# Optimization experiments

Hardware: AMD Instinct MI355X
Metric: run time of the kernel (lower is better)

## Reference

```python
import jax, jax.numpy as jnp
import numpy as np
from jax import lax

DT = 0.001
DX = 0.02
H = 2048
P = 256


def _lap(u):
    # 5-point Laplacian numerator on interior: u[2:,1:-1]-4u[1:-1,1:-1]+u[:-2,1:-1]+u[1:-1,2:]+u[1:-1,:-2]
    return (u[:, :, 2:, 1:-1] - 4.0 * u[:, :, 1:-1, 1:-1] + u[:, :, :-2, 1:-1]
            + u[:, :, 1:-1, 2:] + u[:, :, 1:-1, :-2])


def setup_inputs() -> dict:
    key = jax.random.key(0)
    ks = jax.random.split(key, 8)
    inp = {
        "ref_speed": jax.random.uniform(ks[0], (1, 1, H, H), jnp.float32, 0.1, 1.0),
        "batch": jax.random.normal(ks[1], (12, 1, H, H), jnp.float32),
        "x_tt": jax.random.normal(ks[2], (1, 1, H, H), jnp.float32),
        "x_t": jax.random.normal(ks[3], (1, 1, H, H), jnp.float32),
        "ref_sol": jax.random.normal(ks[4], (16, 1, H, H), jnp.float32),
        "conv_v": jax.random.normal(ks[5], (1, 3, 3, 3), jnp.float32) * np.sqrt(1.0 / (3 * 3 * 320)),
        "conv_g": jax.random.uniform(ks[6], (1,), jnp.float32, 0.5, 1.5),
        "conv_b": jax.random.normal(ks[7], (1,), jnp.float32) * 0.01,
        "loc_x": jax.random.randint(jax.random.fold_in(key, 10), (P,), 0, H),
        "loc_y": jax.random.randint(jax.random.fold_in(key, 11), (P,), 0, H),
        "bsize": 10,
        "id": 1,
        "flag": 1,
        "flag_num": 1,
    }
    return inp


def reference(ref_speed, batch, x_tt, x_t, ref_sol, conv_v, conv_g, conv_b,
              loc_x, loc_y, bsize, id, flag, flag_num):
    sg = lax.stop_gradient
    ntb = flag - 1
    step = flag_num - 1

    xtt = sg(batch[ntb * bsize + step: ntb * bsize + step + 1])   # [1,1,H,W]
    xt = sg(batch[ntb * bsize + step + 1: ntb * bsize + step + 2])

    coef = sg(ref_speed[:, :, 1:-1, 1:-1]) ** 2 * (DT ** 2) / (DX ** 2)

    # explicit FD step (outputs3)
    x_t4 = jnp.zeros_like(xt)
    x_t4 = x_t4.at[:, :, 1:-1, 1:-1].set(
        2.0 * xt[:, :, 1:-1, 1:-1] - xtt[:, :, 1:-1, 1:-1] + _lap(xt) * coef)

    # weight-normed 3x3 conv (3->1 channels, padding=1)
    vnorm = jnp.sqrt(jnp.sum(conv_v ** 2, axis=(1, 2, 3), keepdims=True))
    W = conv_g.reshape(-1, 1, 1, 1) * conv_v / vnorm
    x_t1 = jnp.concatenate([xtt, xt, ref_speed], axis=1)  # [1,3,H,W]
    y = lax.conv_general_dilated(x_t1, W, (1, 1), ((1, 1), (1, 1)),
                                 dimension_numbers=("NCHW", "OIHW", "NCHW"))
    y = y + conv_b.reshape(1, -1, 1, 1)

    # stencil update on conv output interior (RHS evaluated from pre-assignment y)
    x7 = y.at[:, :, 1:-1, 1:-1].set(
        2.0 * xt[:, :, 1:-1, 1:-1] - xtt[:, :, 1:-1, 1:-1] + _lap(y) * coef)
    x7_pre = x7  # clone captured into outputs2 before boundary edits

    # boundaries, in original order
    x7 = x7.at[:, :, 0, :].set(0.0)
    left = xt[:, :, :, 0:1] - DT * sg(ref_speed[:, :, :, 0:1]) * (xt[:, :, :, 0:1] - xt[:, :, :, 1:2]) / DX
    x7 = x7.at[:, :, :, 0:1].set(left)
    rows = jnp.arange(1, H - 1)
    cols = H - rows
    x7 = x7.at[:, :, rows, cols].set(xt[:, :, rows - 1, cols - 1])
    right = xt[:, :, :, -1:] - DT * sg(ref_speed[:, :, :, -1:]) * (xt[:, :, :, -1:] - xt[:, :, :, -2:-1]) / DX
    x7 = x7.at[:, :, :, -1:].set(right)
    x7 = x7.at[:, :, -1, :].set(0.0)

    # per-point observation scatter from ref_sol (-1 entries skipped)
    obs = ref_sol[id * bsize + step + 2: id * bsize + step + 3]  # [1,1,H,W]
    valid = loc_x != -1
    lx = jnp.where(valid, loc_x, 0)
    ly = jnp.where(valid, loc_y, 0)
    vals = obs[:, :, lx, ly]          # [1,1,P]
    cur = x7[:, :, lx, ly]
    x7 = x7.at[:, :, lx, ly].set(jnp.where(valid[None, None, :], vals, cur))

    outputs1 = jnp.concatenate([x_tt, x_t, x7], axis=0)       # [3,1,H,W]
    outputs2 = jnp.concatenate([x_tt, x_t, x7_pre], axis=0)   # [3,1,H,W]
    return jnp.concatenate([outputs1, outputs2, x_t4], axis=0)  # [7,1,H,W]
```

## Files before the change

### kernel.cpp

```cpp
#include <hip/hip_runtime.h>

#define HD   2048
#define HHW  (HD*HD)
#define TX   64
#define TY   32
#define XSTR 68
#define XROWS 36
#define YROWS 34
#define YCOLS 66


__global__ __launch_bounds__(256) void fused_kernel(
    const float* __restrict__ batch,
    const float* __restrict__ rs,
    const float* __restrict__ x_tt_in,
    const float* __restrict__ x_t_in,
    const float* __restrict__ conv_v,
    const float* __restrict__ conv_g,
    const float* __restrict__ conv_b,
    const int* __restrict__ p_bsize,
    const int* __restrict__ p_flag,
    const int* __restrict__ p_flagnum,
    float* __restrict__ out)
{
    __shared__ float xts[XROWS * XSTR];
    __shared__ float ys [YROWS * XSTR];

    const int tid = threadIdx.x;
    const int gi0 = blockIdx.y * TY;
    const int gj0 = blockIdx.x * TX;

    const int base = ((p_flag[0] - 1) * p_bsize[0] + (p_flagnum[0] - 1)) * HHW;
    const float* __restrict__ xtt = batch + base;
    const float* __restrict__ xt  = batch + base + HHW;

    float w[27];
    float ss = 0.f;
    #pragma unroll
    for (int k = 0; k < 27; ++k) { w[k] = conv_v[k]; ss += w[k] * w[k]; }
    const float scale = conv_g[0] / sqrtf(ss);
    const float bias  = conv_b[0];

    for (int p = tid; p < XROWS * XSTR; p += 256) {
        int li = p / XSTR;
        int lj = p - li * XSTR;
        int gi = gi0 - 2 + li;
        int gj = gj0 - 2 + lj;
        float v = 0.f;
        if ((unsigned)gi < HD && (unsigned)gj < HD) v = xt[gi * HD + gj];
        xts[p] = v;
    }
    __syncthreads();

    for (int p = tid; p < YROWS * YCOLS; p += 256) {
        int li = p / YCOLS;
        int lj = p - li * YCOLS;
        int gi = gi0 - 1 + li;
        int gj = gj0 - 1 + lj;
        if ((unsigned)gi >= HD || (unsigned)gj >= HD) continue;
        float acc = 0.f;
        #pragma unroll
        for (int kh = 0; kh < 3; ++kh) {
            int ii = gi + kh - 1;
            bool rok = (unsigned)ii < HD;
            const float* rowt = xtt + ii * HD;
            const float* rowr = rs  + ii * HD;
            #pragma unroll
            for (int kw = 0; kw < 3; ++kw) {
                int jj = gj + kw - 1;
                bool ok = rok && ((unsigned)jj < HD);
                float t0 = ok ? rowt[jj] : 0.f;
                float t1 = xts[(li + kh) * XSTR + lj + kw];
                float t2 = ok ? rowr[jj] : 0.f;
                acc += w[kh * 3 + kw]      * t0
                     + w[9 + kh * 3 + kw]  * t1
                     + w[18 + kh * 3 + kw] * t2;
            }
        }
        ys[li * XSTR + lj] = bias + scale * acc;
    }
    __syncthreads();

    const int c  = tid & 63;
    const int rg = tid >> 6;
    for (int k = 0; k < 8; ++k) {
        int row = rg * 8 + k;
        int gi  = gi0 + row;
        int gj  = gj0 + c;
        int idx = gi * HD + gj;

        float a_tt = x_tt_in[idx];
        float a_t  = x_t_in[idx];
        float xc = xts[(row + 2) * XSTR + c + 2];
        float xo = xtt[idx];
        float rc = rs[idx];
        float yc = ys[(row + 1) * XSTR + c + 1];

        bool interior = (gi > 0) & (gi < HD - 1) & (gj > 0) & (gj < HD - 1);
        float xt4 = 0.f, ypre;
        if (interior) {
            float coef = rc * rc * 0.0025f;
            float lapx = xts[(row + 1) * XSTR + c + 2] + xts[(row + 3) * XSTR + c + 2]
                       + xts[(row + 2) * XSTR + c + 1] + xts[(row + 2) * XSTR + c + 3] - 4.f * xc;
            xt4 = 2.f * xc - xo + lapx * coef;
            float lapy = ys[row * XSTR + c + 1] + ys[(row + 2) * XSTR + c + 1]
                       + ys[(row + 1) * XSTR + c] + ys[(row + 1) * XSTR + c + 2] - 4.f * yc;
            ypre = 2.f * xc - xo + lapy * coef;
        } else {
            ypre = yc;
        }

        float v = ypre;
        if (gi == 0) v = 0.f;
        if (gj == 0)      v = xc - 0.05f * rc * (xc - xts[(row + 2) * XSTR + 3]);
        if (gi >= 1 && gi <= HD - 2 && gj == HD - gi)
                          v = xts[(row + 1) * XSTR + c + 1];
        if (gj == HD - 1) v = xc - 0.05f * rc * (xc - xts[(row + 2) * XSTR + c + 1]);
        if (gi == HD - 1) v = 0.f;

        out[idx]            = a_tt;
        out[HHW + idx]      = a_t;
        out[2 * HHW + idx]  = v;
        out[3 * HHW + idx]  = a_tt;
        out[4 * HHW + idx]  = a_t;
        out[5 * HHW + idx]  = ypre;
        out[6 * HHW + idx]  = xt4;
    }
}

__global__ __launch_bounds__(256) void scatter_kernel(
    const float* __restrict__ ref_sol,
    const int* __restrict__ loc_x,
    const int* __restrict__ loc_y,
    const int* __restrict__ p_bsize,
    const int* __restrict__ p_id,
    const int* __restrict__ p_flagnum,
    float* __restrict__ out)
{
    int k = blockIdx.x * blockDim.x + threadIdx.x;
    if (k >= 256) return;
    int lx = loc_x[k];
    if (lx == -1) return;
    int ly = loc_y[k];
    int off = (p_id[0] * p_bsize[0] + (p_flagnum[0] - 1) + 2) * HHW;
    out[2 * HHW + lx * HD + ly] = ref_sol[off + lx * HD + ly];
}

extern "C" void kernel_launch(void* const* d_in, const int* in_sizes, int n_in,
                              void* d_out, int out_size, void* d_ws, size_t ws_size,
                              hipStream_t stream) {
    const float* ref_speed = (const float*)d_in[0];
    const float* batch     = (const float*)d_in[1];
    const float* x_tt      = (const float*)d_in[2];
    const float* x_t       = (const float*)d_in[3];
    const float* ref_sol   = (const float*)d_in[4];
    const float* conv_v    = (const float*)d_in[5];
    const float* conv_g    = (const float*)d_in[6];
    const float* conv_b    = (const float*)d_in[7];
    const int*   loc_x     = (const int*)d_in[8];
    const int*   loc_y     = (const int*)d_in[9];
    const int*   bsize     = (const int*)d_in[10];
    const int*   id        = (const int*)d_in[11];
    const int*   flag      = (const int*)d_in[12];
    const int*   flag_num  = (const int*)d_in[13];

    float* out = (float*)d_out;

    dim3 block(256);
    dim3 grid(HD / TX, HD / TY);

    fused_kernel<<<grid, block, 0, stream>>>(batch, ref_speed, x_tt, x_t,
                                             conv_v, conv_g, conv_b,
                                             bsize, flag, flag_num, out);
    scatter_kernel<<<1, 256, 0, stream>>>(ref_sol, loc_x, loc_y, bsize, id, flag_num, out);
}
```

Before: 492.1 us.

## Stage all three input tiles in LDS and vectorize with float4

The xtt and ref_speed halo tiles are now staged in shared memory alongside xt, using float4 global loads. The conv and stencil then read only from LDS, and each thread computes four outputs. Output stores also become float4, and launch bounds request 4 blocks per SM. This cuts redundant global reads in the 3x3 conv and improves memory coalescing, at the cost of more LDS per block, which may limit occupancy.

```diff
diff --git a/kernel.cpp b/kernel.cpp
--- a/kernel.cpp
+++ b/kernel.cpp
@@ -4,13 +4,14 @@
 #define HHW  (HD*HD)
 #define TX   64
 #define TY   32
-#define XSTR 68
-#define XROWS 36
-#define YROWS 34
-#define YCOLS 66
-
-
-__global__ __launch_bounds__(256) void fused_kernel(
+#define S    72
+#define XR   36
+#define YR   34
+
+
+union V4 { float4 v; float f[4]; };
+
+__global__ __launch_bounds__(256, 4) void fused_kernel(
     const float* __restrict__ batch,
     const float* __restrict__ rs,
     const float* __restrict__ x_tt_in,
@@ -23,8 +24,10 @@
     const int* __restrict__ p_flagnum,
     float* __restrict__ out)
 {
-    __shared__ float xts[XROWS * XSTR];
-    __shared__ float ys [YROWS * XSTR];
+    __shared__ float sT[XR * S];
+    __shared__ float sX[XR * S];
+    __shared__ float sR[XR * S];
+    __shared__ float sY[YR * S];
 
     const int tid = threadIdx.x;
     const int gi0 = blockIdx.y * TY;
@@ -41,90 +44,142 @@
     const float scale = conv_g[0] / sqrtf(ss);
     const float bias  = conv_b[0];
 
-    for (int p = tid; p < XROWS * XSTR; p += 256) {
-        int li = p / XSTR;
-        int lj = p - li * XSTR;
-        int gi = gi0 - 2 + li;
-        int gj = gj0 - 2 + lj;
-        float v = 0.f;
-        if ((unsigned)gi < HD && (unsigned)gj < HD) v = xt[gi * HD + gj];
-        xts[p] = v;
-    }
+#define STAGE(DST, SRC)                                                     \
+    for (int i = tid; i < XR * 18; i += 256) {                              \
+        const int r  = i / 18;                                              \
+        const int cc = i - r * 18;                                          \
+        const int gi = gi0 - 2 + r;                                         \
+        const int gj = gj0 - 4 + (cc << 2);                                 \
+        float4 val = make_float4(0.f, 0.f, 0.f, 0.f);                       \
+        if ((unsigned)gi < (unsigned)HD && (unsigned)gj <= (unsigned)(HD-4))\
+            val = *(const float4*)(SRC + gi * HD + gj);                     \
+        *(float4*)&DST[r * S + (cc << 2)] = val;                            \
+    }
+
+    STAGE(sT, xtt)
+    STAGE(sX, xt)
+    STAGE(sR, rs)
+#undef STAGE
     __syncthreads();
 
-    for (int p = tid; p < YROWS * YCOLS; p += 256) {
-        int li = p / YCOLS;
-        int lj = p - li * YCOLS;
-        int gi = gi0 - 1 + li;
-        int gj = gj0 - 1 + lj;
-        if ((unsigned)gi >= HD || (unsigned)gj >= HD) continue;
+#define ACC9(SB, WB) {                                                      \
+        V4 a, b, c;                                                         \
+        a.v = *(const float4*)&SB[o - 4];                                   \
+        b.v = *(const float4*)&SB[o];                                       \
+        c.v = *(const float4*)&SB[o + 4];                                   \
+        const float w0 = w[WB], w1 = w[WB + 1], w2 = w[WB + 2];             \
+        ax += w0 * a.f[3] + w1 * b.f[0] + w2 * b.f[1];                      \
+        ay += w0 * b.f[0] + w1 * b.f[1] + w2 * b.f[2];                      \
+        az += w0 * b.f[1] + w1 * b.f[2] + w2 * b.f[3];                      \
+        aw += w0 * b.f[2] + w1 * b.f[3] + w2 * c.f[0];                      \
+    }
+
+    for (int t = tid; t < 34 * 16; t += 256) {
+        const int row = t >> 4;
+        const int ljc = ((t & 15) << 2) + 4;
+        float ax = 0.f, ay = 0.f, az = 0.f, aw = 0.f;
+        #pragma unroll
+        for (int kh = 0; kh < 3; ++kh) {
+            const int o = (row + kh) * S + ljc;
+            ACC9(sT, kh * 3)
+            ACC9(sX, 9 + kh * 3)
+            ACC9(sR, 18 + kh * 3)
+        }
+        V4 r4;
+        r4.f[0] = bias + scale * ax;
+        r4.f[1] = bias + scale * ay;
+        r4.f[2] = bias + scale * az;
+        r4.f[3] = bias + scale * aw;
+        *(float4*)&sY[row * S + ljc] = r4.v;
+    }
+#undef ACC9
+
+    if (tid < 68) {
+        const int row = tid >> 1;
+        const int lj  = (tid & 1) ? 68 : 3;
         float acc = 0.f;
         #pragma unroll
         for (int kh = 0; kh < 3; ++kh) {
-            int ii = gi + kh - 1;
-            bool rok = (unsigned)ii < HD;
-            const float* rowt = xtt + ii * HD;
-            const float* rowr = rs  + ii * HD;
-            #pragma unroll
-            for (int kw = 0; kw < 3; ++kw) {
-                int jj = gj + kw - 1;
-                bool ok = rok && ((unsigned)jj < HD);
-                float t0 = ok ? rowt[jj] : 0.f;
-                float t1 = xts[(li + kh) * XSTR + lj + kw];
-                float t2 = ok ? rowr[jj] : 0.f;
-                acc += w[kh * 3 + kw]      * t0
-                     + w[9 + kh * 3 + kw]  * t1
-                     + w[18 + kh * 3 + kw] * t2;
-            }
+            const int o = (row + kh) * S + lj;
+            acc += w[kh*3+0]      * sT[o-1] + w[kh*3+1]      * sT[o] + w[kh*3+2]      * sT[o+1];
+            acc += w[9+kh*3+0]    * sX[o-1] + w[9+kh*3+1]    * sX[o] + w[9+kh*3+2]    * sX[o+1];
+            acc += w[18+kh*3+0]   * sR[o-1] + w[18+kh*3+1]   * sR[o] + w[18+kh*3+2]   * sR[o+1];
         }
-        ys[li * XSTR + lj] = bias + scale * acc;
+        sY[row * S + lj] = bias + scale * acc;
     }
     __syncthreads();
 
-    const int c  = tid & 63;
-    const int rg = tid >> 6;
-    for (int k = 0; k < 8; ++k) {
-        int row = rg * 8 + k;
-        int gi  = gi0 + row;
-        int gj  = gj0 + c;
-        int idx = gi * HD + gj;
-
-        float a_tt = x_tt_in[idx];
-        float a_t  = x_t_in[idx];
-        float xc = xts[(row + 2) * XSTR + c + 2];
-        float xo = xtt[idx];
-        float rc = rs[idx];
-        float yc = ys[(row + 1) * XSTR + c + 1];
-
-        bool interior = (gi > 0) & (gi < HD - 1) & (gj > 0) & (gj < HD - 1);
-        float xt4 = 0.f, ypre;
-        if (interior) {
-            float coef = rc * rc * 0.0025f;
-            float lapx = xts[(row + 1) * XSTR + c + 2] + xts[(row + 3) * XSTR + c + 2]
-                       + xts[(row + 2) * XSTR + c + 1] + xts[(row + 2) * XSTR + c + 3] - 4.f * xc;
-            xt4 = 2.f * xc - xo + lapx * coef;
-            float lapy = ys[row * XSTR + c + 1] + ys[(row + 2) * XSTR + c + 1]
-                       + ys[(row + 1) * XSTR + c] + ys[(row + 1) * XSTR + c + 2] - 4.f * yc;
-            ypre = 2.f * xc - xo + lapy * coef;
-        } else {
-            ypre = yc;
+    const int c4 = (tid & 15) << 2;
+    const int r0 = tid >> 4;
+    #pragma unroll
+    for (int pass = 0; pass < 2; ++pass) {
+        const int row = r0 + (pass << 4);
+        const int gi  = gi0 + row;
+        const int gjb = gj0 + c4;
+        const int idx = gi * HD + gjb;
+
+        V4 att, at4;
+        att.v = *(const float4*)(x_tt_in + idx);
+        at4.v = *(const float4*)(x_t_in  + idx);
+
+        const int xb = (row + 2) * S + c4 + 4;
+        V4 xc, xu, xd, xl, xr_, xo, rc;
+        xc.v  = *(const float4*)&sX[xb];
+        xu.v  = *(const float4*)&sX[xb - S];
+        xd.v  = *(const float4*)&sX[xb + S];
+        xl.v  = *(const float4*)&sX[xb - 4];
+        xr_.v = *(const float4*)&sX[xb + 4];
+        xo.v  = *(const float4*)&sT[xb];
+        rc.v  = *(const float4*)&sR[xb];
+
+        const int yb = (row + 1) * S + c4 + 4;
+        V4 yc, yu, yd, yl, yr_;
+        yc.v  = *(const float4*)&sY[yb];
+        yu.v  = *(const float4*)&sY[yb - S];
+        yd.v  = *(const float4*)&sY[yb + S];
+        yl.v  = *(const float4*)&sY[yb - 4];
+        yr_.v = *(const float4*)&sY[yb + 4];
+
+        const bool gi_int = (gi >= 1) && (gi <= HD - 2);
+        V4 o2, o5, o6;
+        #pragma unroll
+        for (int e = 0; e < 4; ++e) {
+            const int gj = gjb + e;
+            const float xce  = xc.f[e];
+            const float rce  = rc.f[e];
+            const float xlft = e        ? xc.f[e-1] : xl.f[3];
+            const float xrgt = (e < 3)  ? xc.f[e+1] : xr_.f[0];
+            const float ylft = e        ? yc.f[e-1] : yl.f[3];
+            const float yrgt = (e < 3)  ? yc.f[e+1] : yr_.f[0];
+            const bool interior = gi_int && (gj >= 1) && (gj <= HD - 2);
+
+            const float coef = rce * rce * 0.0025f;
+            const float tm   = 2.f * xce - xo.f[e];
+            const float lapx = xu.f[e] + xd.f[e] + xlft + xrgt - 4.f * xce;
+            const float lapy = yu.f[e] + yd.f[e] + ylft + yrgt - 4.f * yc.f[e];
+
+            float xt4v = 0.f, ypre;
+            if (interior) { xt4v = tm + lapx * coef; ypre = tm + lapy * coef; }
+            else          { ypre = yc.f[e]; }
+
+            float v = ypre;
+            if (gi == 0)            v = 0.f;
+            if (gj == 0)            v = xce - 0.05f * rce * (xce - xrgt);
+            if (gi_int && gj == HD - gi)
+                                    v = sX[(row + 1) * S + c4 + e + 3];
+            if (gj == HD - 1)       v = xce - 0.05f * rce * (xce - xlft);
+            if (gi == HD - 1)       v = 0.f;
+
+            o2.f[e] = v; o5.f[e] = ypre; o6.f[e] = xt4v;
         }
 
-        float v = ypre;
-        if (gi == 0) v = 0.f;
-        if (gj == 0)      v = xc - 0.05f * rc * (xc - xts[(row + 2) * XSTR + 3]);
-        if (gi >= 1 && gi <= HD - 2 && gj == HD - gi)
-                          v = xts[(row + 1) * XSTR + c + 1];
-        if (gj == HD - 1) v = xc - 0.05f * rc * (xc - xts[(row + 2) * XSTR + c + 1]);
-        if (gi == HD - 1) v = 0.f;
-
-        out[idx]            = a_tt;
-        out[HHW + idx]      = a_t;
-        out[2 * HHW + idx]  = v;
-        out[3 * HHW + idx]  = a_tt;
-        out[4 * HHW + idx]  = a_t;
-        out[5 * HHW + idx]  = ypre;
-        out[6 * HHW + idx]  = xt4;
+        *(float4*)(out + idx)           = att.v;
+        *(float4*)(out + HHW + idx)     = at4.v;
+        *(float4*)(out + 2 * HHW + idx) = o2.v;
+        *(float4*)(out + 3 * HHW + idx) = att.v;
+        *(float4*)(out + 4 * HHW + idx) = at4.v;
+        *(float4*)(out + 5 * HHW + idx) = o5.v;
+        *(float4*)(out + 6 * HHW + idx) = o6.v;
     }
 }
 
```

Result: no change. 482.7 us (-1.9%).
